# Performance work log

Hardware: AMD Instinct MI355X
Metric: run time of the kernel (lower is better)

Reference implementation:

```python
import jax, jax.numpy as jnp
import numpy as np

ALPHA = 1.702
LIMIT = 7.0


def setup_inputs() -> dict:
    key = jax.random.key(0)
    ks = jax.random.split(key, 6)
    B, T, H, I, E = 2, 1024, 2048, 2048, 8
    hidden_states = jax.random.normal(ks[0], (B, T, H), dtype=jnp.float32)
    routing_weights = jax.random.uniform(ks[1], (B * T, E), dtype=jnp.float32)
    routing_weights = routing_weights / routing_weights.sum(-1, keepdims=True)
    gate_up_proj = jax.random.normal(ks[2], (E, H, 2 * I), dtype=jnp.float32) * 0.02
    gate_up_proj_bias = jax.random.normal(ks[3], (E, 2 * I), dtype=jnp.float32) * 0.02
    down_proj = jax.random.normal(ks[4], (E, I, H), dtype=jnp.float32) * 0.02
    down_proj_bias = jax.random.normal(ks[5], (E, H), dtype=jnp.float32) * 0.02
    return {
        "hidden_states": hidden_states,
        "routing_weights": routing_weights,
        "gate_up_proj": gate_up_proj,
        "gate_up_proj_bias": gate_up_proj_bias,
        "down_proj": down_proj,
        "down_proj_bias": down_proj_bias,
    }


def reference(hidden_states, routing_weights, gate_up_proj, gate_up_proj_bias,
              down_proj, down_proj_bias):
    # Inference branch of GptOssExperts: dense repeat-all-experts grouped GEMM
    B, T, H = hidden_states.shape
    x = hidden_states.reshape(-1, H)                      # [N, H]
    # [E, N, 2I]
    gate_up = jnp.einsum('nh,ehd->end', x, gate_up_proj) + gate_up_proj_bias[:, None, :]
    gate = gate_up[..., ::2]                              # interleaved split
    up = gate_up[..., 1::2]
    gate = jnp.minimum(gate, LIMIT)
    up = jnp.clip(up, -LIMIT, LIMIT)
    glu = gate * jax.nn.sigmoid(gate * ALPHA)
    # [E, N, H]
    out = jnp.einsum('eni,eih->enh', (up + 1.0) * glu, down_proj) + down_proj_bias[:, None, :]
    out = out * routing_weights.T[..., None]              # weight per (expert, token)
    return out.sum(axis=0).reshape(B, T, H)
```

## Files before the change

### kernel.cpp

```cpp
#include <hip/hip_runtime.h>
#include <cstdint>
#include <cstddef>

#define ALPHA 1.702f
#define LIMIT 7.0f

#define NTOK 2048
#define HDIM 2048
#define IDIM 2048
#define I2   4096
#define NEXP 8

typedef float f32x4 __attribute__((ext_vector_type(4)));
typedef short bf16x8 __attribute__((ext_vector_type(8)));
typedef unsigned short u16;

__device__ __forceinline__ u16 f2bf(float f) {
  unsigned u = __float_as_uint(f);
  u += 0x7fffu + ((u >> 16) & 1u);
  return (u16)(u >> 16);
}

__device__ __forceinline__ void gload_lds16(const void* g, void* l) {
  __builtin_amdgcn_global_load_lds(
      (const __attribute__((address_space(1))) void*)g,
      (__attribute__((address_space(3))) void*)l, 16, 0, 0);
}

#define BARRIER() do { asm volatile("" ::: "memory"); __builtin_amdgcn_s_barrier(); asm volatile("" ::: "memory"); } while (0)
#define VMCNT(n)  asm volatile("s_waitcnt vmcnt(" #n ")" ::: "memory")

__global__ __launch_bounds__(256) void k_cvt(const float* __restrict__ in,
                                             u16* __restrict__ out) {
  int i = blockIdx.x * blockDim.x + threadIdx.x;
  const float4* p = (const float4*)in + (size_t)i * 2;
  float4 a = p[0], b = p[1];
  union { u16 s[8]; uint4 v; } o;
  o.s[0] = f2bf(a.x); o.s[1] = f2bf(a.y); o.s[2] = f2bf(a.z); o.s[3] = f2bf(a.w);
  o.s[4] = f2bf(b.x); o.s[5] = f2bf(b.y); o.s[6] = f2bf(b.z); o.s[7] = f2bf(b.w);
  ((uint4*)out)[i] = o.v;
}

__global__ __launch_bounds__(256) void k_tc(const float* __restrict__ in,
                                            u16* __restrict__ out, int R, int C) {
  __shared__ float tile[64][65];
  const size_t mo = (size_t)blockIdx.z * R * C;
  const float* ip = in + mo;
  u16* op = out + mo;
  const int c0 = blockIdx.x * 64, r0 = blockIdx.y * 64;
  const int t = threadIdx.x;
  const int tr = t >> 4;
  const int tc = (t & 15) * 4;
#pragma unroll
  for (int i = 0; i < 4; ++i) {
    float4 v = *(const float4*)&ip[(size_t)(r0 + tr + i * 16) * C + c0 + tc];
    tile[tr + i * 16][tc] = v.x; tile[tr + i * 16][tc + 1] = v.y;
    tile[tr + i * 16][tc + 2] = v.z; tile[tr + i * 16][tc + 3] = v.w;
  }
  __syncthreads();
  const int cc = t >> 2;
  const int rb = (t & 3) * 8;
#pragma unroll
  for (int i = 0; i < 2; ++i) {
    int r = rb + i * 32;
    union { u16 s[8]; uint4 v; } o;
#pragma unroll
    for (int j = 0; j < 8; ++j) o.s[j] = f2bf(tile[r + j][cc]);
    *(uint4*)&op[(size_t)(c0 + cc) * R + r0 + r] = o.v;
  }
}

#define MFMA_Q(mh, nh, bb) \
  _Pragma("unroll") for (int mm = 0; mm < 4; ++mm) \
  _Pragma("unroll") for (int nn = 0; nn < 2; ++nn) \
  _Pragma("unroll") for (int ks = 0; ks < 2; ++ks) \
    acc[(mh)*4+mm][(nh)*2+nn] = __builtin_amdgcn_mfma_f32_16x16x32_bf16( \
        a[mm][ks], (bb)[nn][ks], acc[(mh)*4+mm][(nh)*2+nn], 0, 0, 0);

__global__ __launch_bounds__(512, 2) void k_gemm1(const u16* __restrict__ xbf,
                                                  const u16* __restrict__ w1t,
                                                  const float* __restrict__ gub,
                                                  const float* __restrict__ rw,
                                                  u16* __restrict__ inter) {
  __shared__ __align__(16) u16 Als[4][128 * 64];
  __shared__ __align__(16) u16 Bls[4][128 * 64];

  const int bid = (int)blockIdx.x;
  const int L = (bid & 7) * 128 + (bid >> 3);
  const int mtile = L & 7, ntile = (L >> 3) & 15, e = L >> 7;
  const int row0 = mtile * 256, col0 = ntile * 256;
  const u16* A = xbf;
  const u16* B = w1t + (size_t)e * I2 * HDIM;

  const int tid = threadIdx.x;
  const int w = tid >> 6, lane = tid & 63;
  const int wr = w >> 2, wc = w & 3;
  const int rrow = lane & 15, klane = lane >> 4;
  const int sA = (wr * 64 + rrow) * 64;
  const int sB = (wc * 32 + rrow) * 64;
  int kofs[2];
  kofs[0] = ((klane ^ (rrow & 7)) << 3);
  kofs[1] = (((4 + klane) ^ (rrow & 7)) << 3);

  auto stA = [&](int reg, int h, int k0) {
#pragma unroll
    for (int j = 0; j < 2; ++j) {
      int c = (w * 2 + j) * 64 + lane;
      int r = c >> 3, gg = c & 7;
      int ksw = ((gg ^ (r & 7)) << 3);
      int R = ((r >> 6) << 7) + h * 64 + (r & 63);
      gload_lds16(A + (size_t)(row0 + R) * HDIM + k0 + ksw,
                  &Als[reg][(size_t)(w * 2 + j) * 512]);
    }
  };
  auto stB = [&](int reg, int h, int k0) {
#pragma unroll
    for (int j = 0; j < 2; ++j) {
      int c = (w * 2 + j) * 64 + lane;
      int r = c >> 3, gg = c & 7;
      int ksw = ((gg ^ (r & 7)) << 3);
      int C = ((r >> 5) << 6) + h * 32 + (r & 31);
      gload_lds16(B + (size_t)(col0 + C) * HDIM + k0 + ksw,
                  &Bls[reg][(size_t)(w * 2 + j) * 512]);
    }
  };

  f32x4 acc[8][4];
#pragma unroll
  for (int i = 0; i < 8; ++i)
#pragma unroll
    for (int j = 0; j < 4; ++j) acc[i][j] = (f32x4){0.f, 0.f, 0.f, 0.f};

  bf16x8 a[4][2], b0[2][2], b1[2][2];
  auto rdA = [&](int reg) {
#pragma unroll
    for (int mm = 0; mm < 4; ++mm)
#pragma unroll
      for (int ks = 0; ks < 2; ++ks)
        a[mm][ks] = *(const bf16x8*)&Als[reg][sA + mm * 1024 + kofs[ks]];
  };
  auto rdB0 = [&](int reg) {
#pragma unroll
    for (int nn = 0; nn < 2; ++nn)
#pragma unroll
      for (int ks = 0; ks < 2; ++ks)
        b0[nn][ks] = *(const bf16x8*)&Bls[reg][sB + nn * 1024 + kofs[ks]];
  };
  auto rdB1 = [&](int reg) {
#pragma unroll
    for (int nn = 0; nn < 2; ++nn)
#pragma unroll
      for (int ks = 0; ks < 2; ++ks)
        b1[nn][ks] = *(const bf16x8*)&Bls[reg][sB + nn * 1024 + kofs[ks]];
  };

  stB(0, 0, 0); stB(1, 1, 0); stA(0, 0, 0); stA(1, 1, 0);
  stB(2, 0, 64); stB(3, 1, 64); stA(2, 0, 64);
  VMCNT(8);
  BARRIER();

  for (int i = 0; i < 16; ++i) {
    const int t = 2 * i;
    const int kA1 = (t + 1) * 64;
    const int kN0 = (t + 2 < 32 ? t + 2 : 31) * 64;
    const int kN1 = (t + 3 < 32 ? t + 3 : 31) * 64;

    rdA(0); rdB0(0);
    stA(3, 1, kA1);
    BARRIER();
    __builtin_amdgcn_s_setprio(1); MFMA_Q(0, 0, b0); __builtin_amdgcn_s_setprio(0);
    BARRIER();

    rdB1(1);
    stB(0, 0, kN0);
    BARRIER();
    __builtin_amdgcn_s_setprio(1); MFMA_Q(0, 1, b1); __builtin_amdgcn_s_setprio(0);
    VMCNT(10);
    BARRIER();

    rdA(1);
    stB(1, 1, kN0);
    BARRIER();
    __builtin_amdgcn_s_setprio(1); MFMA_Q(1, 0, b0); __builtin_amdgcn_s_setprio(0);
    BARRIER();

    stA(0, 0, kN0);
    BARRIER();
    __builtin_amdgcn_s_setprio(1); MFMA_Q(1, 1, b1); __builtin_amdgcn_s_setprio(0);
    VMCNT(8);
    BARRIER();

    rdA(2); rdB0(2);
    stA(1, 1, kN0);
    BARRIER();
    __builtin_amdgcn_s_setprio(1); MFMA_Q(0, 0, b0); __builtin_amdgcn_s_setprio(0);
    BARRIER();

    rdB1(3);
    stB(2, 0, kN1);
    BARRIER();
    __builtin_amdgcn_s_setprio(1); MFMA_Q(0, 1, b1); __builtin_amdgcn_s_setprio(0);
    VMCNT(10);
    BARRIER();

    rdA(3);
    stB(3, 1, kN1);
    BARRIER();
    __builtin_amdgcn_s_setprio(1); MFMA_Q(1, 0, b0); __builtin_amdgcn_s_setprio(0);
    BARRIER();

    stA(2, 0, kN1);
    BARRIER();
    __builtin_amdgcn_s_setprio(1); MFMA_Q(1, 1, b1); __builtin_amdgcn_s_setprio(0);
    VMCNT(8);
    BARRIER();
  }

  const float* bias = gub + (size_t)e * I2;
  u16* ip = inter + (size_t)e * NTOK * IDIM;
#pragma unroll
  for (int ai = 0; ai < 8; ++ai) {
    const int mh = ai >> 2, mm = ai & 3;
#pragma unroll
    for (int bj = 0; bj < 4; ++bj) {
      const int nh = bj >> 1, nn = bj & 1;
      const int col = col0 + wc * 64 + nh * 32 + nn * 16 + rrow;
      const float bv = bias[col];
#pragma unroll
      for (int r = 0; r < 4; ++r) {
        const int row = row0 + wr * 128 + mh * 64 + mm * 16 + klane * 4 + r;
        float gu = acc[ai][bj][r] + bv;
        float pg = __shfl_xor(gu, 1);
        float gate = (lane & 1) ? pg : gu;
        float up   = (lane & 1) ? gu : pg;
        gate = fminf(gate, LIMIT);
        up = fminf(fmaxf(up, -LIMIT), LIMIT);
        float glu = gate / (1.f + __expf(-ALPHA * gate));
        float val = (up + 1.f) * glu * rw[row * NEXP + e];
        if (!(lane & 1)) ip[(size_t)row * IDIM + (col >> 1)] = f2bf(val);
      }
    }
  }
}

__global__ __launch_bounds__(512, 2) void k_gemm2(const u16* __restrict__ inter,
                                                  const u16* __restrict__ w2t,
                                                  float* __restrict__ part) {
  __shared__ __align__(16) u16 Als[4][128 * 64];
  __shared__ __align__(16) u16 Bls[4][128 * 64];

  const int bid = (int)blockIdx.x;
  const int L = (bid & 7) * 32 + (bid >> 3);
  const int mtile = L & 7, ntile = (L >> 3) & 7, sp = L >> 6;
  const int row0 = mtile * 256, col0 = ntile * 256;
  const int es = sp * 2;

  const int tid = threadIdx.x;
  const int w = tid >> 6, lane = tid & 63;
  const int wr = w >> 2, wc = w & 3;
  const int rrow = lane & 15, klane = lane >> 4;
  const int sA = (wr * 64 + rrow) * 64;
  const int sB = (wc * 32 + rrow) * 64;
  int kofs[2];
  kofs[0] = ((klane ^ (rrow & 7)) << 3);
  kofs[1] = (((4 + klane) ^ (rrow & 7)) << 3);

  auto stA = [&](int reg, int h, int k0) {
    const u16* Ab = inter + (size_t)(es + (k0 >> 11)) * NTOK * IDIM;
    const int kk = k0 & 2047;
#pragma unroll
    for (int j = 0; j < 2; ++j) {
      int c = (w * 2 + j) * 64 + lane;
      int r = c >> 3, gg = c & 7;
      int ksw = ((gg ^ (r & 7)) << 3);
      int R = ((r >> 6) << 7) + h * 64 + (r & 63);
      gload_lds16(Ab + (size_t)(row0 + R) * IDIM + kk + ksw,
                  &Als[reg][(size_t)(w * 2 + j) * 512]);
    }
  };
  auto stB = [&](int reg, int h, int k0) {
    const u16* Bb = w2t + (size_t)(es + (k0 >> 11)) * HDIM * IDIM;
    const int kk = k0 & 2047;
#pragma unroll
    for (int j = 0; j < 2; ++j) {
      int c = (w * 2 + j) * 64 + lane;
      int r = c >> 3, gg = c & 7;
      int ksw = ((gg ^ (r & 7)) << 3);
      int C = ((r >> 5) << 6) + h * 32 + (r & 31);
      gload_lds16(Bb + (size_t)(col0 + C) * IDIM + kk + ksw,
                  &Bls[reg][(size_t)(w * 2 + j) * 512]);
    }
  };

  f32x4 acc[8][4];
#pragma unroll
  for (int i = 0; i < 8; ++i)
#pragma unroll
    for (int j = 0; j < 4; ++j) acc[i][j] = (f32x4){0.f, 0.f, 0.f, 0.f};

  bf16x8 a[4][2], b0[2][2], b1[2][2];
  auto rdA = [&](int reg) {
#pragma unroll
    for (int mm = 0; mm < 4; ++mm)
#pragma unroll
      for (int ks = 0; ks < 2; ++ks)
        a[mm][ks] = *(const bf16x8*)&Als[reg][sA + mm * 1024 + kofs[ks]];
  };
  auto rdB0 = [&](int reg) {
#pragma unroll
    for (int nn = 0; nn < 2; ++nn)
#pragma unroll
      for (int ks = 0; ks < 2; ++ks)
        b0[nn][ks] = *(const bf16x8*)&Bls[reg][sB + nn * 1024 + kofs[ks]];
  };
  auto rdB1 = [&](int reg) {
#pragma unroll
    for (int nn = 0; nn < 2; ++nn)
#pragma unroll
      for (int ks = 0; ks < 2; ++ks)
        b1[nn][ks] = *(const bf16x8*)&Bls[reg][sB + nn * 1024 + kofs[ks]];
  };

  stB(0, 0, 0); stB(1, 1, 0); stA(0, 0, 0); stA(1, 1, 0);
  stB(2, 0, 64); stB(3, 1, 64); stA(2, 0, 64);
  VMCNT(8);
  BARRIER();

  for (int i = 0; i < 32; ++i) {
    const int t = 2 * i;
    const int kA1 = (t + 1) * 64;
    const int kN0 = (t + 2 < 64 ? t + 2 : 63) * 64;
    const int kN1 = (t + 3 < 64 ? t + 3 : 63) * 64;

    rdA(0); rdB0(0);
    stA(3, 1, kA1);
    BARRIER();
    __builtin_amdgcn_s_setprio(1); MFMA_Q(0, 0, b0); __builtin_amdgcn_s_setprio(0);
    BARRIER();

    rdB1(1);
    stB(0, 0, kN0);
    BARRIER();
    __builtin_amdgcn_s_setprio(1); MFMA_Q(0, 1, b1); __builtin_amdgcn_s_setprio(0);
    VMCNT(10);
    BARRIER();

    rdA(1);
    stB(1, 1, kN0);
    BARRIER();
    __builtin_amdgcn_s_setprio(1); MFMA_Q(1, 0, b0); __builtin_amdgcn_s_setprio(0);
    BARRIER();

    stA(0, 0, kN0);
    BARRIER();
    __builtin_amdgcn_s_setprio(1); MFMA_Q(1, 1, b1); __builtin_amdgcn_s_setprio(0);
    VMCNT(8);
    BARRIER();

    rdA(2); rdB0(2);
    stA(1, 1, kN0);
    BARRIER();
    __builtin_amdgcn_s_setprio(1); MFMA_Q(0, 0, b0); __builtin_amdgcn_s_setprio(0);
    BARRIER();

    rdB1(3);
    stB(2, 0, kN1);
    BARRIER();
    __builtin_amdgcn_s_setprio(1); MFMA_Q(0, 1, b1); __builtin_amdgcn_s_setprio(0);
    VMCNT(10);
    BARRIER();

    rdA(3);
    stB(3, 1, kN1);
    BARRIER();
    __builtin_amdgcn_s_setprio(1); MFMA_Q(1, 0, b0); __builtin_amdgcn_s_setprio(0);
    BARRIER();

    stA(2, 0, kN1);
    BARRIER();
    __builtin_amdgcn_s_setprio(1); MFMA_Q(1, 1, b1); __builtin_amdgcn_s_setprio(0);
    VMCNT(8);
    BARRIER();
  }

  float* pp = part + (size_t)sp * NTOK * HDIM;
#pragma unroll
  for (int ai = 0; ai < 8; ++ai) {
    const int mh = ai >> 2, mm = ai & 3;
#pragma unroll
    for (int bj = 0; bj < 4; ++bj) {
      const int nh = bj >> 1, nn = bj & 1;
      const int col = col0 + wc * 64 + nh * 32 + nn * 16 + rrow;
#pragma unroll
      for (int r = 0; r < 4; ++r) {
        const int row = row0 + wr * 128 + mh * 64 + mm * 16 + klane * 4 + r;
        pp[(size_t)row * HDIM + col] = acc[ai][bj][r];
      }
    }
  }
}

__global__ __launch_bounds__(256) void k_reduce(const float* __restrict__ part,
                                                const float* __restrict__ dbias,
                                                const float* __restrict__ rw,
                                                float* __restrict__ out) {
  const int i = blockIdx.x * 256 + threadIdx.x;
  const int i4 = i * 4;
  const int n = i4 >> 11;
  const int h = i4 & 2047;
  const size_t MSZ = (size_t)NTOK * HDIM / 4;
  const float4* p = (const float4*)part;
  float4 v0 = p[i];
  float4 v1 = p[i + MSZ];
  float4 v2 = p[i + 2 * MSZ];
  float4 v3 = p[i + 3 * MSZ];
  float4 s;
  s.x = (v0.x + v1.x) + (v2.x + v3.x);
  s.y = (v0.y + v1.y) + (v2.y + v3.y);
  s.z = (v0.z + v1.z) + (v2.z + v3.z);
  s.w = (v0.w + v1.w) + (v2.w + v3.w);
#pragma unroll
  for (int e = 0; e < NEXP; ++e) {
    float rwe = rw[n * NEXP + e];
    float4 db = *(const float4*)&dbias[(size_t)e * HDIM + h];
    s.x += rwe * db.x; s.y += rwe * db.y;
    s.z += rwe * db.z; s.w += rwe * db.w;
  }
  *(float4*)&out[i4] = s;
}

extern "C" void kernel_launch(void* const* d_in, const int* in_sizes, int n_in,
                              void* d_out, int out_size, void* d_ws, size_t ws_size,
                              hipStream_t stream) {
  const float* hs   = (const float*)d_in[0];
  const float* rw   = (const float*)d_in[1];
  const float* gup  = (const float*)d_in[2];
  const float* gupb = (const float*)d_in[3];
  const float* dwn  = (const float*)d_in[4];
  const float* dwnb = (const float*)d_in[5];
  float* out = (float*)d_out;

  u16* xbf   = (u16*)d_ws;
  u16* w1t   = xbf + (size_t)NTOK * HDIM;
  u16* w2t   = w1t + (size_t)NEXP * I2 * HDIM;
  u16* inter = w2t + (size_t)NEXP * HDIM * IDIM;
  float* part = (float*)w1t;
  size_t need = ((size_t)NTOK * HDIM + (size_t)NEXP * I2 * HDIM +
                 (size_t)NEXP * HDIM * IDIM + (size_t)NEXP * NTOK * IDIM) * 2;
  if (ws_size < need) return;

  k_cvt<<<(NTOK * HDIM) / (256 * 8), 256, 0, stream>>>(hs, xbf);

  dim3 g1(I2 / 64, HDIM / 64, NEXP);
  k_tc<<<g1, 256, 0, stream>>>(gup, w1t, HDIM, I2);
  dim3 g2(HDIM / 64, IDIM / 64, NEXP);
  k_tc<<<g2, 256, 0, stream>>>(dwn, w2t, IDIM, HDIM);

  k_gemm1<<<dim3(1024), 512, 0, stream>>>(xbf, w1t, gupb, rw, inter);

  k_gemm2<<<dim3(256), 512, 0, stream>>>(inter, w2t, part);

  k_reduce<<<dim3(NTOK * HDIM / 1024), 256, 0, stream>>>(part, dwnb, rw, out);
}
```

Baseline: 558.9 us.

## Replace pipelined 256x256 gemm1 with simple 128x128 single-buffered kernel

```diff
diff --git a/kernel.cpp b/kernel.cpp
--- a/kernel.cpp
+++ b/kernel.cpp
@@ -70,178 +70,110 @@
   }
 }
 
+__global__ __launch_bounds__(256, 3) void k_gemm1(const u16* __restrict__ xbf,
+                                                  const u16* __restrict__ w1t,
+                                                  const float* __restrict__ gub,
+                                                  const float* __restrict__ rw,
+                                                  u16* __restrict__ inter) {
+  __shared__ __align__(16) u16 As[128 * 32];
+  __shared__ __align__(16) u16 Bs[128 * 32];
+
+  const int bid = (int)blockIdx.x;
+  const int L = (bid & 7) * 512 + (bid >> 3);
+  const int mtile = L & 15, ntile = (L >> 4) & 31, e = L >> 9;
+  const int row0 = mtile * 128, col0 = ntile * 128;
+  const u16* A = xbf;
+  const u16* B = w1t + (size_t)e * I2 * HDIM;
+
+  const int tid = threadIdx.x;
+  const int w = tid >> 6, lane = tid & 63;
+  const int wr = w >> 1, wc = w & 1;
+  const int rrow = lane & 15, klane = lane >> 4;
+  const int kofs = ((klane ^ ((rrow >> 1) & 3)) << 3);
+
+  auto stA = [&](int k0) {
+#pragma unroll
+    for (int j = 0; j < 2; ++j) {
+      int c = (w * 2 + j) * 64 + lane;
+      int r = c >> 2, g = c & 3;
+      int ks = ((g ^ ((r >> 1) & 3)) << 3);
+      gload_lds16(A + (size_t)(row0 + r) * HDIM + k0 + ks,
+                  &As[(size_t)(w * 2 + j) * 512]);
+    }
+  };
+  auto stB = [&](int k0) {
+#pragma unroll
+    for (int j = 0; j < 2; ++j) {
+      int c = (w * 2 + j) * 64 + lane;
+      int r = c >> 2, g = c & 3;
+      int ks = ((g ^ ((r >> 1) & 3)) << 3);
+      gload_lds16(B + (size_t)(col0 + r) * HDIM + k0 + ks,
+                  &Bs[(size_t)(w * 2 + j) * 512]);
+    }
+  };
+
+  f32x4 acc[4][4];
+#pragma unroll
+  for (int m = 0; m < 4; m++)
+#pragma unroll
+    for (int n = 0; n < 4; n++) acc[m][n] = (f32x4){0.f, 0.f, 0.f, 0.f};
+
+  for (int k0 = 0; k0 < HDIM; k0 += 32) {
+    stA(k0); stB(k0);
+    __syncthreads();
+    bf16x8 a[4], b[4];
+#pragma unroll
+    for (int m = 0; m < 4; m++)
+      a[m] = *(const bf16x8*)&As[(wr * 64 + m * 16 + rrow) * 32 + kofs];
+#pragma unroll
+    for (int n = 0; n < 4; n++)
+      b[n] = *(const bf16x8*)&Bs[(wc * 64 + n * 16 + rrow) * 32 + kofs];
+#pragma unroll
+    for (int m = 0; m < 4; m++)
+#pragma unroll
+      for (int n = 0; n < 4; n++)
+        acc[m][n] = __builtin_amdgcn_mfma_f32_16x16x32_bf16(a[m], b[n], acc[m][n], 0, 0, 0);
+    __syncthreads();
+  }
+
+  const float* bias = gub + (size_t)e * I2;
+  u16* ip = inter + (size_t)e * NTOK * IDIM;
+  float bv[4];
+  int cols[4];
+#pragma unroll
+  for (int n = 0; n < 4; n++) {
+    cols[n] = col0 + wc * 64 + n * 16 + rrow;
+    bv[n] = bias[cols[n]];
+  }
+#pragma unroll
+  for (int m = 0; m < 4; m++) {
+#pragma unroll
+    for (int r = 0; r < 4; r++) {
+      int row = row0 + wr * 64 + m * 16 + klane * 4 + r;
+      float wgt = rw[row * NEXP + e];
+#pragma unroll
+      for (int n = 0; n < 4; n++) {
+        float gu = acc[m][n][r] + bv[n];
+        float pg = __shfl_xor(gu, 1);
+        float gate = (lane & 1) ? pg : gu;
+        float up   = (lane & 1) ? gu : pg;
+        gate = fminf(gate, LIMIT);
+        up = fminf(fmaxf(up, -LIMIT), LIMIT);
+        float glu = gate / (1.f + __expf(-ALPHA * gate));
+        float val = (up + 1.f) * glu * wgt;
+        if (!(lane & 1))
+          ip[(size_t)row * IDIM + (cols[n] >> 1)] = f2bf(val);
+      }
+    }
+  }
+}
+
 #define MFMA_Q(mh, nh, bb) \
   _Pragma("unroll") for (int mm = 0; mm < 4; ++mm) \
   _Pragma("unroll") for (int nn = 0; nn < 2; ++nn) \
   _Pragma("unroll") for (int ks = 0; ks < 2; ++ks) \
     acc[(mh)*4+mm][(nh)*2+nn] = __builtin_amdgcn_mfma_f32_16x16x32_bf16( \
         a[mm][ks], (bb)[nn][ks], acc[(mh)*4+mm][(nh)*2+nn], 0, 0, 0);
-
-__global__ __launch_bounds__(512, 2) void k_gemm1(const u16* __restrict__ xbf,
-                                                  const u16* __restrict__ w1t,
-                                                  const float* __restrict__ gub,
-                                                  const float* __restrict__ rw,
-                                                  u16* __restrict__ inter) {
-  __shared__ __align__(16) u16 Als[4][128 * 64];
-  __shared__ __align__(16) u16 Bls[4][128 * 64];
-
-  const int bid = (int)blockIdx.x;
-  const int L = (bid & 7) * 128 + (bid >> 3);
-  const int mtile = L & 7, ntile = (L >> 3) & 15, e = L >> 7;
-  const int row0 = mtile * 256, col0 = ntile * 256;
-  const u16* A = xbf;
-  const u16* B = w1t + (size_t)e * I2 * HDIM;
-
-  const int tid = threadIdx.x;
-  const int w = tid >> 6, lane = tid & 63;
-  const int wr = w >> 2, wc = w & 3;
-  const int rrow = lane & 15, klane = lane >> 4;
-  const int sA = (wr * 64 + rrow) * 64;
-  const int sB = (wc * 32 + rrow) * 64;
-  int kofs[2];
-  kofs[0] = ((klane ^ (rrow & 7)) << 3);
-  kofs[1] = (((4 + klane) ^ (rrow & 7)) << 3);
-
-  auto stA = [&](int reg, int h, int k0) {
-#pragma unroll
-    for (int j = 0; j < 2; ++j) {
-      int c = (w * 2 + j) * 64 + lane;
-      int r = c >> 3, gg = c & 7;
-      int ksw = ((gg ^ (r & 7)) << 3);
-      int R = ((r >> 6) << 7) + h * 64 + (r & 63);
-      gload_lds16(A + (size_t)(row0 + R) * HDIM + k0 + ksw,
-                  &Als[reg][(size_t)(w * 2 + j) * 512]);
-    }
-  };
-  auto stB = [&](int reg, int h, int k0) {
-#pragma unroll
-    for (int j = 0; j < 2; ++j) {
-      int c = (w * 2 + j) * 64 + lane;
-      int r = c >> 3, gg = c & 7;
-      int ksw = ((gg ^ (r & 7)) << 3);
-      int C = ((r >> 5) << 6) + h * 32 + (r & 31);
-      gload_lds16(B + (size_t)(col0 + C) * HDIM + k0 + ksw,
-                  &Bls[reg][(size_t)(w * 2 + j) * 512]);
-    }
-  };
-
-  f32x4 acc[8][4];
-#pragma unroll
-  for (int i = 0; i < 8; ++i)
-#pragma unroll
-    for (int j = 0; j < 4; ++j) acc[i][j] = (f32x4){0.f, 0.f, 0.f, 0.f};
-
-  bf16x8 a[4][2], b0[2][2], b1[2][2];
-  auto rdA = [&](int reg) {
-#pragma unroll
-    for (int mm = 0; mm < 4; ++mm)
-#pragma unroll
-      for (int ks = 0; ks < 2; ++ks)
-        a[mm][ks] = *(const bf16x8*)&Als[reg][sA + mm * 1024 + kofs[ks]];
-  };
-  auto rdB0 = [&](int reg) {
-#pragma unroll
-    for (int nn = 0; nn < 2; ++nn)
-#pragma unroll
-      for (int ks = 0; ks < 2; ++ks)
-        b0[nn][ks] = *(const bf16x8*)&Bls[reg][sB + nn * 1024 + kofs[ks]];
-  };
-  auto rdB1 = [&](int reg) {
-#pragma unroll
-    for (int nn = 0; nn < 2; ++nn)
-#pragma unroll
-      for (int ks = 0; ks < 2; ++ks)
-        b1[nn][ks] = *(const bf16x8*)&Bls[reg][sB + nn * 1024 + kofs[ks]];
-  };
-
-  stB(0, 0, 0); stB(1, 1, 0); stA(0, 0, 0); stA(1, 1, 0);
-  stB(2, 0, 64); stB(3, 1, 64); stA(2, 0, 64);
-  VMCNT(8);
-  BARRIER();
-
-  for (int i = 0; i < 16; ++i) {
-    const int t = 2 * i;
-    const int kA1 = (t + 1) * 64;
-    const int kN0 = (t + 2 < 32 ? t + 2 : 31) * 64;
-    const int kN1 = (t + 3 < 32 ? t + 3 : 31) * 64;
-
-    rdA(0); rdB0(0);
-    stA(3, 1, kA1);
-    BARRIER();
-    __builtin_amdgcn_s_setprio(1); MFMA_Q(0, 0, b0); __builtin_amdgcn_s_setprio(0);
-    BARRIER();
-
-    rdB1(1);
-    stB(0, 0, kN0);
-    BARRIER();
-    __builtin_amdgcn_s_setprio(1); MFMA_Q(0, 1, b1); __builtin_amdgcn_s_setprio(0);
-    VMCNT(10);
-    BARRIER();
-
-    rdA(1);
-    stB(1, 1, kN0);
-    BARRIER();
-    __builtin_amdgcn_s_setprio(1); MFMA_Q(1, 0, b0); __builtin_amdgcn_s_setprio(0);
-    BARRIER();
-
-    stA(0, 0, kN0);
-    BARRIER();
-    __builtin_amdgcn_s_setprio(1); MFMA_Q(1, 1, b1); __builtin_amdgcn_s_setprio(0);
-    VMCNT(8);
-    BARRIER();
-
-    rdA(2); rdB0(2);
-    stA(1, 1, kN0);
-    BARRIER();
-    __builtin_amdgcn_s_setprio(1); MFMA_Q(0, 0, b0); __builtin_amdgcn_s_setprio(0);
-    BARRIER();
-
-    rdB1(3);
-    stB(2, 0, kN1);
-    BARRIER();
-    __builtin_amdgcn_s_setprio(1); MFMA_Q(0, 1, b1); __builtin_amdgcn_s_setprio(0);
-    VMCNT(10);
-    BARRIER();
-
-    rdA(3);
-    stB(3, 1, kN1);
-    BARRIER();
-    __builtin_amdgcn_s_setprio(1); MFMA_Q(1, 0, b0); __builtin_amdgcn_s_setprio(0);
-    BARRIER();
-
-    stA(2, 0, kN1);
-    BARRIER();
-    __builtin_amdgcn_s_setprio(1); MFMA_Q(1, 1, b1); __builtin_amdgcn_s_setprio(0);
-    VMCNT(8);
-    BARRIER();
-  }
-
-  const float* bias = gub + (size_t)e * I2;
-  u16* ip = inter + (size_t)e * NTOK * IDIM;
-#pragma unroll
-  for (int ai = 0; ai < 8; ++ai) {
-    const int mh = ai >> 2, mm = ai & 3;
-#pragma unroll
-    for (int bj = 0; bj < 4; ++bj) {
-      const int nh = bj >> 1, nn = bj & 1;
-      const int col = col0 + wc * 64 + nh * 32 + nn * 16 + rrow;
-      const float bv = bias[col];
-#pragma unroll
-      for (int r = 0; r < 4; ++r) {
-        const int row = row0 + wr * 128 + mh * 64 + mm * 16 + klane * 4 + r;
-        float gu = acc[ai][bj][r] + bv;
-        float pg = __shfl_xor(gu, 1);
-        float gate = (lane & 1) ? pg : gu;
-        float up   = (lane & 1) ? gu : pg;
-        gate = fminf(gate, LIMIT);
-        up = fminf(fmaxf(up, -LIMIT), LIMIT);
-        float glu = gate / (1.f + __expf(-ALPHA * gate));
-        float val = (up + 1.f) * glu * rw[row * NEXP + e];
-        if (!(lane & 1)) ip[(size_t)row * IDIM + (col >> 1)] = f2bf(val);
-      }
-    }
-  }
-}
 
 __global__ __launch_bounds__(512, 2) void k_gemm2(const u16* __restrict__ inter,
                                                   const u16* __restrict__ w2t,
@@ -456,7 +388,7 @@
   dim3 g2(HDIM / 64, IDIM / 64, NEXP);
   k_tc<<<g2, 256, 0, stream>>>(dwn, w2t, IDIM, HDIM);
 
-  k_gemm1<<<dim3(1024), 512, 0, stream>>>(xbf, w1t, gupb, rw, inter);
+  k_gemm1<<<dim3(4096), 256, 0, stream>>>(xbf, w1t, gupb, rw, inter);
 
   k_gemm2<<<dim3(256), 512, 0, stream>>>(inter, w2t, part);
 
```

New measurement: 604.3 us. 8.1% more time.
